# Optimization experiments

Hardware: AMD Instinct MI355X
Metric: run time of the kernel (lower is better)

The kernel has to match this reference:

```python
import jax, jax.numpy as jnp
import numpy as np

# ---- module hyper-params (match init_kwargs) ----
B, C_IN, C_OUT, K, H, W = 16, 128, 128, 3, 56, 56
M, G, STRIDE, RED = 2, 2, 1, 16
R = max(RED, C_IN // RED)            # GC_Attention bottleneck width = 16
MO = M * C_OUT                       # gc_att output channels
GROUPS = G * C_OUT                   # grouped 1x1 fc groups = 256
IN_PG = MO // GROUPS                 # in channels per group = M // G = 1
COUT_FC = C_OUT * C_IN * K * K       # generated weight elements per sample
OUT_PG = COUT_FC // GROUPS           # out channels per group = 576
PAD = K // 2
LN_EPS = 1e-5


def setup_inputs() -> dict:
    key = jax.random.key(0)
    ks = jax.random.split(key, 6)
    sc = 0.05
    return {
        "x": jax.random.normal(ks[0], (B, C_IN, H, W), jnp.float32),
        # GC_Attention: conv_mask (1x1, C->1)
        "w_mask": jax.random.normal(ks[1], (C_IN,), jnp.float32) * sc,
        "b_mask": jnp.zeros((), jnp.float32),
        # transform: conv1x1 C->R, LayerNorm(R), ReLU, conv1x1 R->M*out
        "w1": jax.random.normal(ks[2], (R, C_IN), jnp.float32) * sc,
        "b1": jnp.zeros((R,), jnp.float32),
        "ln_g": jnp.ones((R,), jnp.float32),
        "ln_b": jnp.zeros((R,), jnp.float32),
        "w2": jax.random.normal(ks[3], (MO, R), jnp.float32) * sc,
        "b2": jnp.zeros((MO,), jnp.float32),
        # fc: grouped 1x1 conv, groups=G*out, stored [groups, out_pg, in_pg]
        "w_fc": jax.random.normal(ks[4], (GROUPS, OUT_PG, IN_PG), jnp.float32) * sc,
        "b_fc": jnp.zeros((COUT_FC,), jnp.float32),
    }


def reference(x, w_mask, b_mask, w1, b1, ln_g, ln_b, w2, b2, w_fc, b_fc):
    b, c, h, w = x.shape
    # --- GC_Attention: global-context pooling via spatial softmax ---
    mask = jnp.einsum('bchw,c->bhw', x, w_mask) + b_mask        # [b,h,w]
    att = jax.nn.softmax(mask.reshape(b, -1), axis=-1)          # [b,hw]
    ctx = jnp.einsum('bcs,bs->bc', x.reshape(b, c, -1), att)    # [b,C]
    # bottleneck transform (1x1 convs on [b,*,1,1] == dense layers)
    t = ctx @ w1.T + b1                                          # [b,R]
    mu = t.mean(-1, keepdims=True)
    var = t.var(-1, keepdims=True)
    t = (t - mu) / jnp.sqrt(var + LN_EPS) * ln_g + ln_b          # LayerNorm over R
    t = jax.nn.relu(t)
    a = jax.nn.sigmoid(t @ w2.T + b2)                            # [b, M*out]
    # --- grouped 1x1 conv: generate per-sample conv weights ---
    xw = jnp.einsum('bgi,goi->bgo', a.reshape(b, GROUPS, IN_PG), w_fc)
    xw = xw.reshape(b, COUT_FC) + b_fc
    Wd = xw.reshape(b, C_OUT, C_IN, K, K)                        # per-sample kernels
    # --- per-sample conv2d (torch: groups=b on batch-folded input) ---
    def conv1(xi, wi):
        return jax.lax.conv_general_dilated(
            xi[None], wi, (STRIDE, STRIDE), [(PAD, PAD), (PAD, PAD)],
            dimension_numbers=('NCHW', 'OIHW', 'NCHW'))[0]
    return jax.vmap(conv1)(x, Wd)                                # [b, out, H, W]
```

## Files before the change

### kernel.cpp

```cpp
#include <hip/hip_runtime.h>
#include <hip/hip_bf16.h>
#include <math.h>

#define BATCH 16
#define CIN   128
#define COUT  128
#define SS    3136
#define XT_ROW 8192
#define XT_PER_B (58*XT_ROW)
#define NKB   18

typedef __attribute__((ext_vector_type(8))) __bf16 bf16x8;
typedef __attribute__((ext_vector_type(4))) float  floatx4;

static __device__ __forceinline__ unsigned short f2bf(float f) {
  union { float f; unsigned u; } v; v.f = f;
  unsigned r = v.u + 0x7fffu + ((v.u >> 16) & 1u);
  return (unsigned short)(r >> 16);
}
static __device__ __forceinline__ float bf2f(unsigned short u) {
  union { unsigned u; float f; } v; v.u = ((unsigned)u) << 16; return v.f;
}

static __device__ __forceinline__ float waveReduceSum(float v) {
  #pragma unroll
  for (int off = 32; off > 0; off >>= 1) v += __shfl_xor(v, off, 64);
  return v;
}

static __device__ __forceinline__ void load_lds16(const void* g, void* l) {
  __builtin_amdgcn_global_load_lds(
      (const __attribute__((address_space(1))) void*)g,
      (__attribute__((address_space(3))) void*)l, 16, 0, 0);
}

static __device__ __forceinline__ int sswz(int ci) {
  return (ci ^ (ci >> 4)) & 15;
}

__global__ __launch_bounds__(256, 4)
void k0_padT(const float* __restrict__ x, const float* __restrict__ w_mask,
             const float* __restrict__ b_mask,
             unsigned short* __restrict__ xT, float* __restrict__ rowsum,
             float* __restrict__ pctx) {
  int b = blockIdx.y, prow = blockIdx.x, t = threadIdx.x;
  int y = prow - 1;
  __shared__ __align__(16) unsigned short sx[128 * 64];
  __shared__ float swm[128];
  __shared__ float red[4 * 56];
  __shared__ float se[56];
  bool rowvalid = ((unsigned)y < 56u);

  if (!rowvalid) {
    unsigned short* dst = xT + (size_t)(b * 58 + prow) * XT_ROW;
    uint4 z4 = make_uint4(0u, 0u, 0u, 0u);
    #pragma unroll
    for (int q = 0; q < 4; q++)
      *reinterpret_cast<uint4*>(dst + (size_t)(t + 256 * q) * 8) = z4;
    if (t == 0) rowsum[b * 58 + prow] = 0.f;
    if (t < 128) pctx[(size_t)(b * 58 + prow) * 128 + t] = 0.f;
    return;
  }

  if (t < 128) swm[t] = w_mask[t];
  #pragma unroll
  for (int i = 0; i < 7; i++) {
    int c = t + 256 * i;
    int ci = c / 14, j = c - ci * 14;
    const float4 v = *reinterpret_cast<const float4*>(
        x + (size_t)(b * 128 + ci) * SS + y * 56 + j * 4);
    union { unsigned short s[4]; uint2 u; } pk;
    pk.s[0] = f2bf(v.x); pk.s[1] = f2bf(v.y);
    pk.s[2] = f2bf(v.z); pk.s[3] = f2bf(v.w);
    int blk = j ^ sswz(ci);
    *reinterpret_cast<uint2*>(&sx[ci * 64 + (blk << 2)]) = pk.u;
  }
  __syncthreads();

  if (t < 224) {
    int xx = t % 56, g = t / 56;
    float acc = 0.f;
    #pragma unroll
    for (int k = 0; k < 32; k++) {
      int ci = g * 32 + k;
      acc += bf2f(sx[ci * 64 + ((((xx >> 2) ^ sswz(ci)) << 2) | (xx & 3))]) * swm[ci];
    }
    red[g * 56 + xx] = acc;
  }
  __syncthreads();

  float e = 0.f;
  if (t < 56) {
    float m = red[t] + red[56 + t] + red[112 + t] + red[168 + t] + b_mask[0];
    e = expf(m);
    se[t] = e;
  }
  if (t < 64) {
    float s = waveReduceSum(e);
    if (t == 0) rowsum[b * 58 + prow] = s;
  }

  {
    int pcol = t >> 2, cig = t & 3;
    int xx = pcol - 1;
    bool colv = ((unsigned)xx < 56u);
    unsigned short tmp[32];
    #pragma unroll
    for (int i = 0; i < 32; i++) {
      int ci = cig * 32 + i;
      tmp[i] = colv ? sx[ci * 64 + ((((xx >> 2) ^ sswz(ci)) << 2) | (xx & 3))]
                    : (unsigned short)0;
    }
    unsigned short* dst = xT + ((size_t)(b * 58 + prow) * 64 + pcol) * 128 + cig * 32;
    #pragma unroll
    for (int q = 0; q < 4; q++)
      *reinterpret_cast<uint4*>(dst + q * 8) = *reinterpret_cast<const uint4*>(tmp + q * 8);
  }
  __syncthreads();

  {
    int c = t >> 1, h = t & 1;
    float acc = 0.f;
    #pragma unroll
    for (int j = 0; j < 28; j++) {
      int col = h * 28 + j;
      acc += bf2f(sx[c * 64 + ((((col >> 2) ^ sswz(c)) << 2) | (col & 3))]) * se[col];
    }
    acc += __shfl_xor(acc, 1, 64);
    if (h == 0) pctx[(size_t)(b * 58 + prow) * 128 + c] = acc;
  }
}

__global__ void k4_mlp(const float* __restrict__ rowsum, float* __restrict__ pctx,
                       const float* __restrict__ w1, const float* __restrict__ b1,
                       const float* __restrict__ ln_g, const float* __restrict__ ln_b,
                       const float* __restrict__ w2, const float* __restrict__ b2) {
  int b = blockIdx.x, t = threadIdx.x;
  __shared__ float sc[128], st[16], sn[16], shz;
  float rv = (t < 58) ? rowsum[b * 58 + t] : 0.f;
  float acc = 0.f;
  #pragma unroll
  for (int r = 0; r < 58; r++) acc += pctx[(size_t)(b * 58 + r) * 128 + t];
  if (t < 64) {
    float z = waveReduceSum(rv);
    if (t == 0) shz = 1.0f / z;
  }
  __syncthreads();
  sc[t] = acc * shz;
  __syncthreads();
  if (t < 16) {
    float s = b1[t];
    #pragma unroll 8
    for (int c = 0; c < 128; c++) s += sc[c] * w1[t * 128 + c];
    st[t] = s;
  }
  __syncthreads();
  if (t < 16) {
    float mu = 0.f, m2 = 0.f;
    #pragma unroll
    for (int r = 0; r < 16; r++) { float v = st[r]; mu += v; m2 += v * v; }
    mu *= (1.f / 16.f); m2 *= (1.f / 16.f);
    float rstd = rsqrtf(m2 - mu * mu + 1e-5f);
    float v = (st[t] - mu) * rstd * ln_g[t] + ln_b[t];
    sn[t] = fmaxf(v, 0.f);
  }
  __syncthreads();
  #pragma unroll
  for (int k = 0; k < 2; k++) {
    int mo = t + 128 * k;
    float s = b2[mo];
    #pragma unroll
    for (int r = 0; r < 16; r++) s += sn[r] * w2[mo * 16 + r];
    pctx[(size_t)b * (58 * 128) + mo] = 1.f / (1.f + expf(-s));
  }
}

__global__ void k5_wgen(const float* __restrict__ w_fc, const float* __restrict__ b_fc,
                        const float* __restrict__ abuf, unsigned short* __restrict__ wd) {
  int co = blockIdx.x, bp = blockIdx.y, t = threadIdx.x;
  int ci = t & 127, bb = t >> 7, b = bp * 2 + bb;
  __shared__ unsigned short sw[2][1152];
  const float* wr = w_fc + co * 1152 + ci * 9;
  const float* br = b_fc + co * 1152 + ci * 9;
  float a = abuf[(size_t)b * (58 * 128) + 2 * co + (ci >> 6)];
  int kq = ci & 63;
  int pos = (((kq >> 3) ^ (co & 7)) << 3) | (kq & 7);
  int kb0 = ci >> 6;
  #pragma unroll
  for (int khw = 0; khw < 9; khw++) {
    float v = a * wr[khw] + br[khw];
    sw[bb][(khw * 2 + kb0) * 64 + pos] = f2bf(v);
  }
  __syncthreads();
  for (int c = t; c < 288; c += 256) {
    int row = c / 144, q = c - row * 144;
    unsigned short* dst = wd + (size_t)((bp * 2 + row) * 128 + co) * 1152 + q * 8;
    *reinterpret_cast<uint4*>(dst) = *reinterpret_cast<const uint4*>(&sw[row][q * 8]);
  }
}

__global__ __launch_bounds__(512, 4) void k6_conv(const unsigned short* __restrict__ xT,
                                                  const unsigned short* __restrict__ wd,
                                                  float* __restrict__ out) {
  __shared__ __align__(16) unsigned short As[8192];
  __shared__ __align__(16) unsigned short Bs[8192];
  int t = threadIdx.x;
  int b = blockIdx.y, y0 = blockIdx.x * 2;
  int wave = t >> 6, lane = t & 63, l15 = lane & 15, quad = lane >> 4;
  int x7 = lane & 7;
  const unsigned short* wp  = wd + (size_t)b * (128 * 1152);
  const unsigned short* xTb = xT + (size_t)b * XT_PER_B;

  int ch0 = wave * 128 + lane, ch1 = ch0 + 64;
  int offA0 = (ch0 >> 3) * 1152 + (ch0 & 7) * 8;
  int offA1 = (ch1 >> 3) * 1152 + (ch1 & 7) * 8;
  int s0 = ch0 >> 3, s1 = ch1 >> 3;
  int c_ = lane & 7;
  int sr0 = s0 / 56, sc0 = s0 - sr0 * 56; if (sr0 >= 2) { sr0 = 0; sc0 = 0; }
  int sr1 = s1 / 56, sc1 = s1 - sr1 * 56; if (sr1 >= 2) { sr1 = 0; sc1 = 0; }
  int offB0 = (y0 + sr0) * XT_ROW + sc0 * 128 + (c_ ^ (s0 & 7)) * 8;
  int offB1 = (y0 + sr1) * XT_ROW + sc1 * 128 + (c_ ^ (s1 & 7)) * 8;
  unsigned short* dA0 = &As[wave * 1024];
  unsigned short* dA1 = &As[wave * 1024 + 512];
  unsigned short* dB0 = &Bs[wave * 1024];
  unsigned short* dB1 = &Bs[wave * 1024 + 512];

  int s_base = (wave & 3) * 32;
  int co_b   = (wave >> 2) * 64;

  floatx4 acc[4][2];
  floatx4 zero = {0.f, 0.f, 0.f, 0.f};
  #pragma unroll
  for (int i = 0; i < 4; i++)
    #pragma unroll
    for (int j = 0; j < 2; j++) acc[i][j] = zero;

  for (int kb = 0; kb < NKB; kb++) {
    int khw = kb >> 1;
    int kh = khw / 3;
    int kw = khw - kh * 3;
    int dB = kh * XT_ROW + kw * 128 + ((kb & 1) << 6);
    int dA = kb * 64;
    __syncthreads();
    load_lds16(wp + offA0 + dA, dA0);
    load_lds16(wp + offA1 + dA, dA1);
    load_lds16(xTb + offB0 + dB, dB0);
    load_lds16(xTb + offB1 + dB, dB1);
    __syncthreads();
    #pragma unroll
    for (int kk = 0; kk < 2; kk++) {
      bf16x8 af[4], bfr[2];
      int pc = ((kk * 4 + quad) ^ x7) << 3;
      #pragma unroll
      for (int i = 0; i < 4; i++)
        af[i] = *reinterpret_cast<const bf16x8*>(&As[(co_b + i * 16 + l15) * 64 + pc]);
      #pragma unroll
      for (int j = 0; j < 2; j++)
        bfr[j] = *reinterpret_cast<const bf16x8*>(&Bs[(s_base + j * 16 + l15) * 64 + pc]);
      #pragma unroll
      for (int i = 0; i < 4; i++)
        #pragma unroll
        for (int j = 0; j < 2; j++)
          acc[i][j] = __builtin_amdgcn_mfma_f32_16x16x32_bf16(af[i], bfr[j], acc[i][j], 0, 0, 0);
    }
  }

  float* ob = out + (size_t)b * COUT * SS + y0 * 56;
  #pragma unroll
  for (int i = 0; i < 4; i++) {
    #pragma unroll
    for (int j = 0; j < 2; j++) {
      int sl = s_base + j * 16 + l15;
      if (sl < 112) {
        int row = (sl >= 56) ? 1 : 0;
        int col = sl - row * 56;
        #pragma unroll
        for (int r = 0; r < 4; r++) {
          int co = co_b + i * 16 + quad * 4 + r;
          ob[(size_t)co * SS + row * 56 + col] = acc[i][j][r];
        }
      }
    }
  }
}

extern "C" void kernel_launch(void* const* d_in, const int* in_sizes, int n_in,
                              void* d_out, int out_size, void* d_ws, size_t ws_size,
                              hipStream_t stream) {
  const float* x      = (const float*)d_in[0];
  const float* w_mask = (const float*)d_in[1];
  const float* b_mask = (const float*)d_in[2];
  const float* w1     = (const float*)d_in[3];
  const float* b1     = (const float*)d_in[4];
  const float* ln_g   = (const float*)d_in[5];
  const float* ln_b   = (const float*)d_in[6];
  const float* w2     = (const float*)d_in[7];
  const float* b2     = (const float*)d_in[8];
  const float* w_fc   = (const float*)d_in[9];
  const float* b_fc   = (const float*)d_in[10];
  float* out = (float*)d_out;

  char* ws = (char*)d_ws;
  unsigned short* xT  = (unsigned short*)(ws);
  unsigned short* wdw = (unsigned short*)(ws + 15204352);
  float* rowsum = (float*)(ws + 19922944);
  float* pctx   = (float*)(ws + 19927040);

  k0_padT<<<dim3(58, 16),  dim3(256), 0, stream>>>(x, w_mask, b_mask, xT, rowsum, pctx);
  k4_mlp <<<dim3(16),      dim3(128), 0, stream>>>(rowsum, pctx, w1, b1, ln_g, ln_b, w2, b2);
  k5_wgen<<<dim3(128, 8),  dim3(256), 0, stream>>>(w_fc, b_fc, pctx, wdw);
  k6_conv<<<dim3(28, 16),  dim3(512), 0, stream>>>(xT, wdw, out);
}
```

Measured before the change: 132.7 us.

## Double-buffer LDS tiles in conv kernel to overlap loads with MFMA

```diff
diff --git a/kernel.cpp b/kernel.cpp
--- a/kernel.cpp
+++ b/kernel.cpp
@@ -32,6 +32,12 @@
   __builtin_amdgcn_global_load_lds(
       (const __attribute__((address_space(1))) void*)g,
       (__attribute__((address_space(3))) void*)l, 16, 0, 0);
+}
+
+static __device__ __forceinline__ void barrier_fenced() {
+  asm volatile("" ::: "memory");
+  __builtin_amdgcn_s_barrier();
+  asm volatile("" ::: "memory");
 }
 
 static __device__ __forceinline__ int sswz(int ci) {
@@ -202,8 +208,8 @@
 __global__ __launch_bounds__(512, 4) void k6_conv(const unsigned short* __restrict__ xT,
                                                   const unsigned short* __restrict__ wd,
                                                   float* __restrict__ out) {
-  __shared__ __align__(16) unsigned short As[8192];
-  __shared__ __align__(16) unsigned short Bs[8192];
+  __shared__ __align__(16) unsigned short As[2][8192];
+  __shared__ __align__(16) unsigned short Bs[2][8192];
   int t = threadIdx.x;
   int b = blockIdx.y, y0 = blockIdx.x * 2;
   int wave = t >> 6, lane = t & 63, l15 = lane & 15, quad = lane >> 4;
@@ -220,10 +226,6 @@
   int sr1 = s1 / 56, sc1 = s1 - sr1 * 56; if (sr1 >= 2) { sr1 = 0; sc1 = 0; }
   int offB0 = (y0 + sr0) * XT_ROW + sc0 * 128 + (c_ ^ (s0 & 7)) * 8;
   int offB1 = (y0 + sr1) * XT_ROW + sc1 * 128 + (c_ ^ (s1 & 7)) * 8;
-  unsigned short* dA0 = &As[wave * 1024];
-  unsigned short* dA1 = &As[wave * 1024 + 512];
-  unsigned short* dB0 = &Bs[wave * 1024];
-  unsigned short* dB1 = &Bs[wave * 1024 + 512];
 
   int s_base = (wave & 3) * 32;
   int co_b   = (wave >> 2) * 64;
@@ -235,34 +237,47 @@
     #pragma unroll
     for (int j = 0; j < 2; j++) acc[i][j] = zero;
 
-  for (int kb = 0; kb < NKB; kb++) {
+  auto stage = [&](int buf, int kb) {
     int khw = kb >> 1;
     int kh = khw / 3;
     int kw = khw - kh * 3;
     int dB = kh * XT_ROW + kw * 128 + ((kb & 1) << 6);
     int dA = kb * 64;
-    __syncthreads();
-    load_lds16(wp + offA0 + dA, dA0);
-    load_lds16(wp + offA1 + dA, dA1);
-    load_lds16(xTb + offB0 + dB, dB0);
-    load_lds16(xTb + offB1 + dB, dB1);
-    __syncthreads();
+    load_lds16(wp + offA0 + dA, &As[buf][wave * 1024]);
+    load_lds16(wp + offA1 + dA, &As[buf][wave * 1024 + 512]);
+    load_lds16(xTb + offB0 + dB, &Bs[buf][wave * 1024]);
+    load_lds16(xTb + offB1 + dB, &Bs[buf][wave * 1024 + 512]);
+  };
+
+  stage(0, 0);
+  for (int kb = 0; kb < NKB; kb++) {
+    int cur = kb & 1;
+    if (kb + 1 < NKB) {
+      stage(cur ^ 1, kb + 1);
+      asm volatile("s_waitcnt vmcnt(4)" ::: "memory");
+    } else {
+      asm volatile("s_waitcnt vmcnt(0)" ::: "memory");
+    }
+    barrier_fenced();
+    __builtin_amdgcn_s_setprio(1);
     #pragma unroll
     for (int kk = 0; kk < 2; kk++) {
       bf16x8 af[4], bfr[2];
       int pc = ((kk * 4 + quad) ^ x7) << 3;
       #pragma unroll
       for (int i = 0; i < 4; i++)
-        af[i] = *reinterpret_cast<const bf16x8*>(&As[(co_b + i * 16 + l15) * 64 + pc]);
+        af[i] = *reinterpret_cast<const bf16x8*>(&As[cur][(co_b + i * 16 + l15) * 64 + pc]);
       #pragma unroll
       for (int j = 0; j < 2; j++)
-        bfr[j] = *reinterpret_cast<const bf16x8*>(&Bs[(s_base + j * 16 + l15) * 64 + pc]);
+        bfr[j] = *reinterpret_cast<const bf16x8*>(&Bs[cur][(s_base + j * 16 + l15) * 64 + pc]);
       #pragma unroll
       for (int i = 0; i < 4; i++)
         #pragma unroll
         for (int j = 0; j < 2; j++)
           acc[i][j] = __builtin_amdgcn_mfma_f32_16x16x32_bf16(af[i], bfr[j], acc[i][j], 0, 0, 0);
     }
+    __builtin_amdgcn_s_setprio(0);
+    barrier_fenced();
   }
 
   float* ob = out + (size_t)b * COUT * SS + y0 * 56;
```

Measured after the change: 132.7 us. Within noise of the previous version (-0.0%).
